# Kernel optimization log

Hardware: AMD Instinct MI355X
Metric: run time of the kernel (lower is better)

Reference implementation:

```python
import jax, jax.numpy as jnp
import numpy as np

N, C, H, W = 2, 128, 64, 256
GROUPS, S = 8, 9  # 3x3 search window


def setup_inputs() -> dict:
    key = jax.random.key(0)
    k1, k2, k3 = jax.random.split(key, 3)
    left = jax.random.normal(k1, (N, C, H, W), jnp.float32)
    right = jax.random.normal(k2, (N, C, H, W), jnp.float32)
    # per-pixel learned offsets: (N, S*2, H, W), reshaped to (N,S,2,H,W) inside
    extra_offset = jax.random.normal(k3, (N, S * 2, H, W), jnp.float32)
    return {"left_feature": left, "right_feature": right, "extra_offset": extra_offset}


def _bilinear_sample(im, x, y):
    """im: (N,C,H,W); x,y: (N,L) pixel coords. Zero padding outside borders
    (matches bilinear_grid_sample: 1-px zero pad + index clamp into pad)."""
    n, c, h, w = im.shape
    x0f = jnp.floor(x)
    y0f = jnp.floor(y)
    x1f = x0f + 1.0
    y1f = y0f + 1.0
    wa = (x1f - x) * (y1f - y)
    wb = (x1f - x) * (y - y0f)
    wc = (x - x0f) * (y1f - y)
    wd = (x - x0f) * (y - y0f)
    ph, pw = h + 2, w + 2
    im_p = jnp.pad(im, ((0, 0), (0, 0), (1, 1), (1, 1))).reshape(n, c, ph * pw)
    x0 = jnp.clip(x0f.astype(jnp.int32) + 1, 0, pw - 1)
    x1 = jnp.clip(x1f.astype(jnp.int32) + 1, 0, pw - 1)
    y0 = jnp.clip(y0f.astype(jnp.int32) + 1, 0, ph - 1)
    y1 = jnp.clip(y1f.astype(jnp.int32) + 1, 0, ph - 1)

    def g(xi, yi):
        idx = (xi + yi * pw)[:, None, :]  # (N,1,L) -> broadcast over C
        return jnp.take_along_axis(im_p, idx, axis=2)

    out = (g(x0, y0) * wa[:, None, :] + g(x0, y1) * wb[:, None, :]
           + g(x1, y0) * wc[:, None, :] + g(x1, y1) * wd[:, None, :])
    return out  # (N,C,L)


def reference(left_feature, right_feature, extra_offset):
    n, c, h, w = left_feature.shape
    cg = c // GROUPS
    # base 3x3 offsets, (x,y) pairs in torch meshgrid 'ij' order
    r = jnp.arange(-1, 2, dtype=jnp.float32)
    xg, yg = jnp.meshgrid(r, r, indexing='ij')
    base = jnp.stack([xg, yg], axis=-1).reshape(S, 2)  # (9,2)
    eo = extra_offset.reshape(n, S, 2, h, w).transpose(0, 1, 3, 4, 2)  # (N,S,H,W,2)
    off = base[None, :, None, None, :] + eo
    gx = jnp.arange(w, dtype=jnp.float32)
    gy = jnp.arange(h, dtype=jnp.float32)
    x = (off[..., 0] + gx[None, None, None, :]).reshape(n, -1)  # (N, S*H*W)
    y = (off[..., 1] + gy[None, None, :, None]).reshape(n, -1)
    # offsets are shared across groups -> sample all channels once
    sampled = _bilinear_sample(right_feature, x, y).reshape(n, GROUPS, cg, S, h, w)
    left_g = left_feature.reshape(n, GROUPS, cg, 1, h, w)
    corr = jnp.mean(left_g * sampled, axis=2)  # (N, GROUPS, S, H, W)
    return corr.reshape(n, GROUPS * S, h, w)
```

## Files before the change

### kernel.cpp

```cpp
#include <hip/hip_runtime.h>
#include <stdint.h>


#define NB 2
#define CC 128
#define HH 64
#define WW 256
#define GG 8
#define CG 16
#define SS 9
#define HW (HH * WW)
#define TY 4
#define RW 5
#define NSLOT 16
#define HALFDW 1056
#define SLOTQ (2 * HALFDW)
#define SMEMDW (NSLOT * SLOTQ)

typedef __fp16 h2v __attribute__((ext_vector_type(2)));

static __device__ __forceinline__ uint32_t pkrtz(float a, float b) {
    h2v v = __builtin_amdgcn_cvt_pkrtz(a, b);
    return __builtin_bit_cast(uint32_t, v);
}
static __device__ __forceinline__ h2v u2h(uint32_t u) {
    return __builtin_bit_cast(h2v, u);
}

#if __has_builtin(__builtin_amdgcn_fdot2)
#define FDOT2(A, B, C) __builtin_amdgcn_fdot2((A), (B), (C), false)
#else
#define FDOT2(A, B, C) fmaf((float)(A).x, (float)(B).x, \
                            fmaf((float)(A).y, (float)(B).y, (C)))
#endif

#define DOT16(LOP, RES)                                                        \
  {                                                                            \
    const uint4 u0_ = *(const uint4*)(LOP);                                    \
    const uint4 u1_ = *(const uint4*)((LOP) + HALFDW);                         \
    RES = FDOT2(u2h(u0_.x), u2h(lvpk[0]),                                      \
          FDOT2(u2h(u0_.y), u2h(lvpk[1]),                                      \
          FDOT2(u2h(u0_.z), u2h(lvpk[2]),                                      \
          FDOT2(u2h(u0_.w), u2h(lvpk[3]),                                      \
          FDOT2(u2h(u1_.x), u2h(lvpk[4]),                                      \
          FDOT2(u2h(u1_.y), u2h(lvpk[5]),                                      \
          FDOT2(u2h(u1_.z), u2h(lvpk[6]),                                      \
          FDOT2(u2h(u1_.w), u2h(lvpk[7]), 0.0f))))))));                        \
  }

__global__ __launch_bounds__(1024) void corr_kernel(
    const float* __restrict__ left, const float* __restrict__ right,
    const float* __restrict__ eo, float* __restrict__ out)
{
    __shared__ uint32_t smem[SMEMDW];

    const int tid = threadIdx.x;
    const int lane = tid & 63;
    const int wv = tid >> 6;
    const int bid = blockIdx.x;
    const int g = bid & (GG - 1);
    const int h0 = ((bid >> 3) & 15) << 2;
    const int n = bid >> 7;
    const int gch = g * CG;

    const int virt_row0 = h0 - RW;
    const int row0 = max(0, virt_row0);
    const int row_last = min(HH - 1, h0 + TY + RW - 1);
    const int nrows = row_last - row0 + 1;
    const int sbase = row0 - virt_row0 + 1;

    const int hh = tid >> 8;
    const int h = h0 + hh;
    const int wcol = tid & 255;
    const int pix = h * WW + wcol;

    const float* rnb = right + (size_t)n * CC * HW;
    const float* lp  = left  + (size_t)(n * CC + gch) * HW + pix;
    const float* eob = eo + (size_t)n * SS * 2 * HW + pix;

    for (int i = tid; i < SMEMDW / 4; i += 1024)
        *(uint4*)&smem[4 * i] = make_uint4(0u, 0u, 0u, 0u);
    __syncthreads();

#pragma unroll
    for (int pass = 0; pass < 4; ++pass) {
        if (wv < nrows) {
            const int cq = 64 * pass + lane;
            const float* s0 = rnb + (size_t)gch * HW + (row0 + wv) * WW + cq;
            uint32_t pk8[8];
#pragma unroll
            for (int p = 0; p < 8; ++p)
                pk8[p] = pkrtz(s0[(size_t)(2 * p) * HW],
                               s0[(size_t)(2 * p + 1) * HW]);
            uint32_t* dst = &smem[(sbase + wv) * SLOTQ + 4 * (cq + 1)];
            *(uint4*)dst            = make_uint4(pk8[0], pk8[1], pk8[2], pk8[3]);
            *(uint4*)(dst + HALFDW) = make_uint4(pk8[4], pk8[5], pk8[6], pk8[7]);
        }
    }

    uint32_t lvpk[8];
#pragma unroll
    for (int p = 0; p < 8; ++p)
        lvpk[p] = pkrtz(lp[(size_t)(2 * p) * HW], lp[(size_t)(2 * p + 1) * HW]);

    __syncthreads();

    float acc[SS];
#pragma unroll
    for (int s = 0; s < SS; ++s) acc[s] = 0.0f;

#pragma unroll
    for (int s = 0; s < SS; ++s) {
        const float x = (float)(s / 3 - 1) + eob[(2 * s) * HW] + (float)wcol;
        const float y = (float)(s % 3 - 1) + eob[(2 * s + 1) * HW] + (float)h;
        const float x0f = floorf(x), y0f = floorf(y);
        const float fx0 = x - x0f, fx1 = 1.0f - fx0;
        const float fy0 = y - y0f, fy1 = 1.0f - fy0;
        const int x0 = (int)x0f, y0 = (int)y0f;
        const int x1 = x0 + 1,   y1 = y0 + 1;
        const bool vx0 = (unsigned)x0 < (unsigned)WW;
        const bool vx1 = (unsigned)x1 < (unsigned)WW;
        const bool vy0 = (unsigned)y0 < (unsigned)HH;
        const bool vy1 = (unsigned)y1 < (unsigned)HH;
        const float wA = (vx0 && vy0) ? fx1 * fy1 : 0.0f;
        const float wB = (vx1 && vy0) ? fx0 * fy1 : 0.0f;
        const float wC = (vx0 && vy1) ? fx1 * fy0 : 0.0f;
        const float wD = (vx1 && vy1) ? fx0 * fy0 : 0.0f;

        const bool bad = (vy0 && (y0 < row0 || y0 > row_last)) ||
                         (vy1 && (y1 < row0 || y1 > row_last));

        if (__builtin_expect(!bad, 1)) {
            const int xc = min(max(x0, -1), WW);
            const int rr = min(max(y0 - virt_row0 + 1, 0), NSLOT - 2);
            const uint32_t* rp0 = smem + rr * SLOTQ + 4 * (xc + 1);
            const uint32_t* rp1 = rp0 + SLOTQ;
            float dA, dB, dC, dD;
            DOT16(rp0,     dA)
            DOT16(rp0 + 4, dB)
            DOT16(rp1,     dC)
            DOT16(rp1 + 4, dD)
            acc[s] += fmaf(wA, dA, fmaf(wB, dB, fmaf(wC, dC, wD * dD)));
        } else {
            const int cx0 = min(max(x0, 0), WW - 1), cx1 = min(max(x1, 0), WW - 1);
            const int cy0 = min(max(y0, 0), HH - 1), cy1 = min(max(y1, 0), HH - 1);
#pragma unroll
            for (int p = 0; p < 8; ++p) {
                const h2v lv = u2h(lvpk[p]);
#pragma unroll
                for (int c2 = 0; c2 < 2; ++c2) {
                    const float* rp2 = rnb + (size_t)(gch + 2 * p + c2) * HW;
                    const float v = wA * rp2[cy0 * WW + cx0] + wB * rp2[cy0 * WW + cx1]
                                  + wC * rp2[cy1 * WW + cx0] + wD * rp2[cy1 * WW + cx1];
                    acc[s] += (c2 ? (float)lv.y : (float)lv.x) * v;
                }
            }
        }
    }

    float* ob = out + ((size_t)(n * GG + g) * SS) * HW + pix;
#pragma unroll
    for (int s = 0; s < SS; ++s)
        ob[s * HW] = acc[s] * (1.0f / CG);
}

extern "C" void kernel_launch(void* const* d_in, const int* in_sizes, int n_in,
                              void* d_out, int out_size, void* d_ws, size_t ws_size,
                              hipStream_t stream) {
    const float* left  = (const float*)d_in[0];
    const float* right = (const float*)d_in[1];
    const float* eo    = (const float*)d_in[2];
    float* out = (float*)d_out;
    (void)d_ws; (void)ws_size; (void)in_sizes; (void)n_in; (void)out_size;

    dim3 grid(NB * (HH / TY) * GG);
    dim3 block(1024);
    corr_kernel<<<grid, block, 0, stream>>>(left, right, eo, out);
}
```

Before: 21.14 us.

## Split channel halves to overlap second-half smem staging with first-half compute

Stages only the first 8 channels of the right feature rows into shared memory before the first barrier. While computing the 9 displacements on that half, it interleaves global loads and smem stores of the second 8-channel half. The second half is then computed after another barrier. The aim is to hide global-load latency behind compute. The cost is recomputing the bilinear coordinates and weights twice and doing two eo loads per displacement.

```diff
diff --git a/kernel.cpp b/kernel.cpp
--- a/kernel.cpp
+++ b/kernel.cpp
@@ -34,18 +34,78 @@
                             fmaf((float)(A).y, (float)(B).y, (C)))
 #endif
 
-#define DOT16(LOP, RES)                                                        \
+#define DOT8(P, L0, L1, L2, L3, RES)                                           \
   {                                                                            \
-    const uint4 u0_ = *(const uint4*)(LOP);                                    \
-    const uint4 u1_ = *(const uint4*)((LOP) + HALFDW);                         \
-    RES = FDOT2(u2h(u0_.x), u2h(lvpk[0]),                                      \
-          FDOT2(u2h(u0_.y), u2h(lvpk[1]),                                      \
-          FDOT2(u2h(u0_.z), u2h(lvpk[2]),                                      \
-          FDOT2(u2h(u0_.w), u2h(lvpk[3]),                                      \
-          FDOT2(u2h(u1_.x), u2h(lvpk[4]),                                      \
-          FDOT2(u2h(u1_.y), u2h(lvpk[5]),                                      \
-          FDOT2(u2h(u1_.z), u2h(lvpk[6]),                                      \
-          FDOT2(u2h(u1_.w), u2h(lvpk[7]), 0.0f))))))));                        \
+    const uint4 u_ = *(const uint4*)(P);                                       \
+    RES = FDOT2(u2h(u_.x), u2h(L0),                                            \
+          FDOT2(u2h(u_.y), u2h(L1),                                            \
+          FDOT2(u2h(u_.z), u2h(L2),                                            \
+          FDOT2(u2h(u_.w), u2h(L3), 0.0f))));                                  \
+  }
+
+#define SHALF(S, PHALF, CHB, L0, L1, L2, L3)                                   \
+  {                                                                            \
+    const float x = (float)((S) / 3 - 1) + eob[(2 * (S)) * HW] + (float)wcol;  \
+    const float y = (float)((S) % 3 - 1) + eob[(2 * (S) + 1) * HW] + (float)h; \
+    const float x0f = floorf(x), y0f = floorf(y);                              \
+    const float fx0 = x - x0f, fx1 = 1.0f - fx0;                               \
+    const float fy0 = y - y0f, fy1 = 1.0f - fy0;                               \
+    const int x0 = (int)x0f, y0 = (int)y0f;                                    \
+    const int x1 = x0 + 1, y1 = y0 + 1;                                        \
+    const bool vx0 = (unsigned)x0 < (unsigned)WW;                              \
+    const bool vx1 = (unsigned)x1 < (unsigned)WW;                              \
+    const bool vy0 = (unsigned)y0 < (unsigned)HH;                              \
+    const bool vy1 = (unsigned)y1 < (unsigned)HH;                              \
+    const float wA = (vx0 && vy0) ? fx1 * fy1 : 0.0f;                          \
+    const float wB = (vx1 && vy0) ? fx0 * fy1 : 0.0f;                          \
+    const float wC = (vx0 && vy1) ? fx1 * fy0 : 0.0f;                          \
+    const float wD = (vx1 && vy1) ? fx0 * fy0 : 0.0f;                          \
+    const bool bad = (vy0 && (y0 < row0 || y0 > row_last)) ||                  \
+                     (vy1 && (y1 < row0 || y1 > row_last));                    \
+    if (__builtin_expect(!bad, 1)) {                                           \
+      const int xc = min(max(x0, -1), WW);                                     \
+      const int rr = min(max(y0 - virt_row0 + 1, 0), NSLOT - 2);               \
+      const uint32_t* rp0 = smem + rr * SLOTQ + (PHALF) + 4 * (xc + 1);        \
+      const uint32_t* rp1 = rp0 + SLOTQ;                                       \
+      float dA, dB, dC, dD;                                                    \
+      DOT8(rp0,     L0, L1, L2, L3, dA)                                        \
+      DOT8(rp0 + 4, L0, L1, L2, L3, dB)                                        \
+      DOT8(rp1,     L0, L1, L2, L3, dC)                                        \
+      DOT8(rp1 + 4, L0, L1, L2, L3, dD)                                        \
+      acc[S] += fmaf(wA, dA, fmaf(wB, dB, fmaf(wC, dC, wD * dD)));             \
+    } else {                                                                   \
+      const int cx0 = min(max(x0, 0), WW - 1), cx1 = min(max(x1, 0), WW - 1);  \
+      const int cy0 = min(max(y0, 0), HH - 1), cy1 = min(max(y1, 0), HH - 1);  \
+      _Pragma("unroll")                                                        \
+      for (int p_ = 0; p_ < 4; ++p_) {                                         \
+        const h2v lvp_ = (p_ == 0) ? u2h(L0) : (p_ == 1) ? u2h(L1)             \
+                        : (p_ == 2) ? u2h(L2) : u2h(L3);                       \
+        _Pragma("unroll")                                                      \
+        for (int c2_ = 0; c2_ < 2; ++c2_) {                                    \
+          const float* rq_ = rnb + (size_t)(gch + (CHB) + 2 * p_ + c2_) * HW;  \
+          const float v_ = wA * rq_[cy0 * WW + cx0] + wB * rq_[cy0 * WW + cx1] \
+                         + wC * rq_[cy1 * WW + cx0] + wD * rq_[cy1 * WW + cx1];\
+          acc[S] += (c2_ ? (float)lvp_.y : (float)lvp_.x) * v_;                \
+        }                                                                      \
+      }                                                                        \
+    }                                                                          \
+  }
+
+#define SLOAD(PASS, CHB)                                                       \
+  if (wv < nrows) {                                                            \
+    const int cq_ = 64 * (PASS) + lane;                                        \
+    const float* s0_ = rnb + (size_t)(gch + (CHB)) * HW                        \
+                     + (row0 + wv) * WW + cq_;                                 \
+    f0 = s0_[0];      f1 = s0_[HW];     f2 = s0_[2 * HW]; f3 = s0_[3 * HW];    \
+    f4 = s0_[4 * HW]; f5 = s0_[5 * HW]; f6 = s0_[6 * HW]; f7 = s0_[7 * HW];    \
+  }
+
+#define SSTORE(PASS, PHALF)                                                    \
+  if (wv < nrows) {                                                            \
+    const int cq_ = 64 * (PASS) + lane;                                        \
+    uint32_t* d_ = &smem[(sbase + wv) * SLOTQ + (PHALF) + 4 * (cq_ + 1)];      \
+    *(uint4*)d_ = make_uint4(pkrtz(f0, f1), pkrtz(f2, f3),                     \
+                             pkrtz(f4, f5), pkrtz(f6, f7));                    \
   }
 
 __global__ __launch_bounds__(1024) void corr_kernel(
@@ -82,81 +142,59 @@
         *(uint4*)&smem[4 * i] = make_uint4(0u, 0u, 0u, 0u);
     __syncthreads();
 
+    float f0, f1, f2, f3, f4, f5, f6, f7;
+
 #pragma unroll
     for (int pass = 0; pass < 4; ++pass) {
-        if (wv < nrows) {
-            const int cq = 64 * pass + lane;
-            const float* s0 = rnb + (size_t)gch * HW + (row0 + wv) * WW + cq;
-            uint32_t pk8[8];
-#pragma unroll
-            for (int p = 0; p < 8; ++p)
-                pk8[p] = pkrtz(s0[(size_t)(2 * p) * HW],
-                               s0[(size_t)(2 * p + 1) * HW]);
-            uint32_t* dst = &smem[(sbase + wv) * SLOTQ + 4 * (cq + 1)];
-            *(uint4*)dst            = make_uint4(pk8[0], pk8[1], pk8[2], pk8[3]);
-            *(uint4*)(dst + HALFDW) = make_uint4(pk8[4], pk8[5], pk8[6], pk8[7]);
-        }
+        SLOAD(pass, 0)
+        SSTORE(pass, 0)
     }
 
-    uint32_t lvpk[8];
-#pragma unroll
-    for (int p = 0; p < 8; ++p)
-        lvpk[p] = pkrtz(lp[(size_t)(2 * p) * HW], lp[(size_t)(2 * p + 1) * HW]);
-
-    __syncthreads();
+    uint32_t lv0, lv1, lv2, lv3, lv4, lv5, lv6, lv7;
+    lv0 = pkrtz(lp[0],          lp[(size_t)1 * HW]);
+    lv1 = pkrtz(lp[(size_t)2 * HW],  lp[(size_t)3 * HW]);
+    lv2 = pkrtz(lp[(size_t)4 * HW],  lp[(size_t)5 * HW]);
+    lv3 = pkrtz(lp[(size_t)6 * HW],  lp[(size_t)7 * HW]);
+    lv4 = pkrtz(lp[(size_t)8 * HW],  lp[(size_t)9 * HW]);
+    lv5 = pkrtz(lp[(size_t)10 * HW], lp[(size_t)11 * HW]);
+    lv6 = pkrtz(lp[(size_t)12 * HW], lp[(size_t)13 * HW]);
+    lv7 = pkrtz(lp[(size_t)14 * HW], lp[(size_t)15 * HW]);
 
     float acc[SS];
 #pragma unroll
     for (int s = 0; s < SS; ++s) acc[s] = 0.0f;
 
-#pragma unroll
-    for (int s = 0; s < SS; ++s) {
-        const float x = (float)(s / 3 - 1) + eob[(2 * s) * HW] + (float)wcol;
-        const float y = (float)(s % 3 - 1) + eob[(2 * s + 1) * HW] + (float)h;
-        const float x0f = floorf(x), y0f = floorf(y);
-        const float fx0 = x - x0f, fx1 = 1.0f - fx0;
-        const float fy0 = y - y0f, fy1 = 1.0f - fy0;
-        const int x0 = (int)x0f, y0 = (int)y0f;
-        const int x1 = x0 + 1,   y1 = y0 + 1;
-        const bool vx0 = (unsigned)x0 < (unsigned)WW;
-        const bool vx1 = (unsigned)x1 < (unsigned)WW;
-        const bool vy0 = (unsigned)y0 < (unsigned)HH;
-        const bool vy1 = (unsigned)y1 < (unsigned)HH;
-        const float wA = (vx0 && vy0) ? fx1 * fy1 : 0.0f;
-        const float wB = (vx1 && vy0) ? fx0 * fy1 : 0.0f;
-        const float wC = (vx0 && vy1) ? fx1 * fy0 : 0.0f;
-        const float wD = (vx1 && vy1) ? fx0 * fy0 : 0.0f;
-
-        const bool bad = (vy0 && (y0 < row0 || y0 > row_last)) ||
-                         (vy1 && (y1 < row0 || y1 > row_last));
-
-        if (__builtin_expect(!bad, 1)) {
-            const int xc = min(max(x0, -1), WW);
-            const int rr = min(max(y0 - virt_row0 + 1, 0), NSLOT - 2);
-            const uint32_t* rp0 = smem + rr * SLOTQ + 4 * (xc + 1);
-            const uint32_t* rp1 = rp0 + SLOTQ;
-            float dA, dB, dC, dD;
-            DOT16(rp0,     dA)
-            DOT16(rp0 + 4, dB)
-            DOT16(rp1,     dC)
-            DOT16(rp1 + 4, dD)
-            acc[s] += fmaf(wA, dA, fmaf(wB, dB, fmaf(wC, dC, wD * dD)));
-        } else {
-            const int cx0 = min(max(x0, 0), WW - 1), cx1 = min(max(x1, 0), WW - 1);
-            const int cy0 = min(max(y0, 0), HH - 1), cy1 = min(max(y1, 0), HH - 1);
-#pragma unroll
-            for (int p = 0; p < 8; ++p) {
-                const h2v lv = u2h(lvpk[p]);
-#pragma unroll
-                for (int c2 = 0; c2 < 2; ++c2) {
-                    const float* rp2 = rnb + (size_t)(gch + 2 * p + c2) * HW;
-                    const float v = wA * rp2[cy0 * WW + cx0] + wB * rp2[cy0 * WW + cx1]
-                                  + wC * rp2[cy1 * WW + cx0] + wD * rp2[cy1 * WW + cx1];
-                    acc[s] += (c2 ? (float)lv.y : (float)lv.x) * v;
-                }
-            }
-        }
-    }
+    __syncthreads();
+
+    SLOAD(0, 8)
+    SHALF(0, 0, 0, lv0, lv1, lv2, lv3)
+    SHALF(1, 0, 0, lv0, lv1, lv2, lv3)
+    SHALF(2, 0, 0, lv0, lv1, lv2, lv3)
+    SSTORE(0, HALFDW)
+    SLOAD(1, 8)
+    SHALF(3, 0, 0, lv0, lv1, lv2, lv3)
+    SHALF(4, 0, 0, lv0, lv1, lv2, lv3)
+    SHALF(5, 0, 0, lv0, lv1, lv2, lv3)
+    SSTORE(1, HALFDW)
+    SLOAD(2, 8)
+    SHALF(6, 0, 0, lv0, lv1, lv2, lv3)
+    SHALF(7, 0, 0, lv0, lv1, lv2, lv3)
+    SHALF(8, 0, 0, lv0, lv1, lv2, lv3)
+    SSTORE(2, HALFDW)
+    SLOAD(3, 8)
+    SSTORE(3, HALFDW)
+
+    __syncthreads();
+
+    SHALF(0, HALFDW, 8, lv4, lv5, lv6, lv7)
+    SHALF(1, HALFDW, 8, lv4, lv5, lv6, lv7)
+    SHALF(2, HALFDW, 8, lv4, lv5, lv6, lv7)
+    SHALF(3, HALFDW, 8, lv4, lv5, lv6, lv7)
+    SHALF(4, HALFDW, 8, lv4, lv5, lv6, lv7)
+    SHALF(5, HALFDW, 8, lv4, lv5, lv6, lv7)
+    SHALF(6, HALFDW, 8, lv4, lv5, lv6, lv7)
+    SHALF(7, HALFDW, 8, lv4, lv5, lv6, lv7)
+    SHALF(8, HALFDW, 8, lv4, lv5, lv6, lv7)
 
     float* ob = out + ((size_t)(n * GG + g) * SS) * HW + pix;
 #pragma unroll
```

Measured after the change: 25.36 us. 20.0% more time.

## Overlap offset and left loads with staging; precompute sample addresses before barrier

Applied to the files above, without the earlier changes.

The kernel now zeroes only unstaged shared-memory slots and the pad cells of staged ones, instead of clearing the whole buffer. The offset and left-feature global loads are issued before the first barrier, and all bilinear addresses and weights are computed before the second barrier, so this latency overlaps with staging. Weights are packed to fp16 pairs to save registers, and each output is stored right after its dot product. The fp16 weights reduce accuracy slightly, and the rare fallback path recomputes coordinates from global memory.

```diff
diff --git a/kernel.cpp b/kernel.cpp
--- a/kernel.cpp
+++ b/kernel.cpp
@@ -78,8 +78,30 @@
     const float* lp  = left  + (size_t)(n * CC + gch) * HW + pix;
     const float* eob = eo + (size_t)n * SS * 2 * HW + pix;
 
-    for (int i = tid; i < SMEMDW / 4; i += 1024)
-        *(uint4*)&smem[4 * i] = make_uint4(0u, 0u, 0u, 0u);
+    {
+        const bool staged = (wv >= sbase) && (wv < sbase + nrows);
+        uint32_t* slot = &smem[wv * SLOTQ];
+        if (!staged) {
+            for (int i = lane; i < SLOTQ / 4; i += 64)
+                *(uint4*)&slot[4 * i] = make_uint4(0u, 0u, 0u, 0u);
+        } else if (lane < 16) {
+            const int half = lane >> 3;
+            const int cellsel = (lane >> 2) & 1;
+            const int dwi = lane & 3;
+            slot[half * HALFDW + cellsel * (257 * 4) + dwi] = 0u;
+        }
+    }
+
+    float eox[SS], eoy[SS];
+#pragma unroll
+    for (int s = 0; s < SS; ++s) {
+        eox[s] = eob[(2 * s) * HW];
+        eoy[s] = eob[(2 * s + 1) * HW];
+    }
+    float lf[CG];
+#pragma unroll
+    for (int c = 0; c < CG; ++c) lf[c] = lp[(size_t)c * HW];
+
     __syncthreads();
 
 #pragma unroll
@@ -101,18 +123,15 @@
     uint32_t lvpk[8];
 #pragma unroll
     for (int p = 0; p < 8; ++p)
-        lvpk[p] = pkrtz(lp[(size_t)(2 * p) * HW], lp[(size_t)(2 * p + 1) * HW]);
-
-    __syncthreads();
-
-    float acc[SS];
-#pragma unroll
-    for (int s = 0; s < SS; ++s) acc[s] = 0.0f;
-
+        lvpk[p] = pkrtz(lf[2 * p], lf[2 * p + 1]);
+
+    int lbase[SS];
+    uint32_t wab[SS], wcd[SS];
+    int badmask = 0;
 #pragma unroll
     for (int s = 0; s < SS; ++s) {
-        const float x = (float)(s / 3 - 1) + eob[(2 * s) * HW] + (float)wcol;
-        const float y = (float)(s % 3 - 1) + eob[(2 * s + 1) * HW] + (float)h;
+        const float x = (float)(s / 3 - 1) + eox[s] + (float)wcol;
+        const float y = (float)(s % 3 - 1) + eoy[s] + (float)h;
         const float x0f = floorf(x), y0f = floorf(y);
         const float fx0 = x - x0f, fx1 = 1.0f - fx0;
         const float fy0 = y - y0f, fy1 = 1.0f - fy0;
@@ -126,42 +145,67 @@
         const float wB = (vx1 && vy0) ? fx0 * fy1 : 0.0f;
         const float wC = (vx0 && vy1) ? fx1 * fy0 : 0.0f;
         const float wD = (vx1 && vy1) ? fx0 * fy0 : 0.0f;
-
-        const bool bad = (vy0 && (y0 < row0 || y0 > row_last)) ||
-                         (vy1 && (y1 < row0 || y1 > row_last));
-
-        if (__builtin_expect(!bad, 1)) {
-            const int xc = min(max(x0, -1), WW);
-            const int rr = min(max(y0 - virt_row0 + 1, 0), NSLOT - 2);
-            const uint32_t* rp0 = smem + rr * SLOTQ + 4 * (xc + 1);
+        wab[s] = pkrtz(wA, wB);
+        wcd[s] = pkrtz(wC, wD);
+        const int xc = min(max(x0, -1), WW);
+        const int rr = min(max(y0 - virt_row0 + 1, 0), NSLOT - 2);
+        lbase[s] = rr * SLOTQ + 4 * (xc + 1);
+        if ((vy0 && (y0 < row0 || y0 > row_last)) ||
+            (vy1 && (y1 < row0 || y1 > row_last)))
+            badmask |= 1 << s;
+    }
+
+    __syncthreads();
+
+    float* ob = out + ((size_t)(n * GG + g) * SS) * HW + pix;
+
+#pragma unroll
+    for (int s = 0; s < SS; ++s) {
+        float val;
+        if (__builtin_expect(!((badmask >> s) & 1), 1)) {
+            const uint32_t* rp0 = smem + lbase[s];
             const uint32_t* rp1 = rp0 + SLOTQ;
             float dA, dB, dC, dD;
             DOT16(rp0,     dA)
             DOT16(rp0 + 4, dB)
             DOT16(rp1,     dC)
             DOT16(rp1 + 4, dD)
-            acc[s] += fmaf(wA, dA, fmaf(wB, dB, fmaf(wC, dC, wD * dD)));
+            const h2v w01 = u2h(wab[s]), w23 = u2h(wcd[s]);
+            val = fmaf((float)w01.x, dA, fmaf((float)w01.y, dB,
+                  fmaf((float)w23.x, dC, (float)w23.y * dD)));
         } else {
+            const float x = (float)(s / 3 - 1) + eob[(2 * s) * HW] + (float)wcol;
+            const float y = (float)(s % 3 - 1) + eob[(2 * s + 1) * HW] + (float)h;
+            const float x0f = floorf(x), y0f = floorf(y);
+            const float fx0 = x - x0f, fx1 = 1.0f - fx0;
+            const float fy0 = y - y0f, fy1 = 1.0f - fy0;
+            const int x0 = (int)x0f, y0 = (int)y0f;
+            const int x1 = x0 + 1,   y1 = y0 + 1;
+            const bool vx0 = (unsigned)x0 < (unsigned)WW;
+            const bool vx1 = (unsigned)x1 < (unsigned)WW;
+            const bool vy0 = (unsigned)y0 < (unsigned)HH;
+            const bool vy1 = (unsigned)y1 < (unsigned)HH;
+            const float a = (vx0 && vy0) ? fx1 * fy1 : 0.0f;
+            const float b = (vx1 && vy0) ? fx0 * fy1 : 0.0f;
+            const float c3 = (vx0 && vy1) ? fx1 * fy0 : 0.0f;
+            const float d = (vx1 && vy1) ? fx0 * fy0 : 0.0f;
             const int cx0 = min(max(x0, 0), WW - 1), cx1 = min(max(x1, 0), WW - 1);
             const int cy0 = min(max(y0, 0), HH - 1), cy1 = min(max(y1, 0), HH - 1);
+            val = 0.0f;
 #pragma unroll
             for (int p = 0; p < 8; ++p) {
                 const h2v lv = u2h(lvpk[p]);
 #pragma unroll
                 for (int c2 = 0; c2 < 2; ++c2) {
                     const float* rp2 = rnb + (size_t)(gch + 2 * p + c2) * HW;
-                    const float v = wA * rp2[cy0 * WW + cx0] + wB * rp2[cy0 * WW + cx1]
-                                  + wC * rp2[cy1 * WW + cx0] + wD * rp2[cy1 * WW + cx1];
-                    acc[s] += (c2 ? (float)lv.y : (float)lv.x) * v;
+                    const float v = a * rp2[cy0 * WW + cx0] + b * rp2[cy0 * WW + cx1]
+                                  + c3 * rp2[cy1 * WW + cx0] + d * rp2[cy1 * WW + cx1];
+                    val += (c2 ? (float)lv.y : (float)lv.x) * v;
                 }
             }
         }
-    }
-
-    float* ob = out + ((size_t)(n * GG + g) * SS) * HW + pix;
-#pragma unroll
-    for (int s = 0; s < SS; ++s)
-        ob[s * HW] = acc[s] * (1.0f / CG);
+        ob[s * HW] = val * (1.0f / CG);
+    }
 }
 
 extern "C" void kernel_launch(void* const* d_in, const int* in_sizes, int n_in,
```

Result: slower. 24.27 us (+14.8%).
